# Performance work log

Hardware: AMD Instinct MI355X
Metric: run time of the kernel (lower is better)

Reference implementation:

```python
import jax, jax.numpy as jnp
import numpy as np
from jax import lax

N_NODES = 100_000
N_EDGES = 1_600_000
IN_CH = 128


def setup_inputs():
    key = jax.random.key(0)
    kx, ks, kd, kw, kb = jax.random.split(key, 5)
    x = jax.random.normal(kx, (N_NODES, IN_CH), dtype=jnp.float32)
    src = jax.random.randint(ks, (N_EDGES,), 0, N_NODES)
    dst = jax.random.randint(kd, (N_EDGES,), 0, N_NODES)
    # symmetrize (undirected graph, as PyG datasets typically are)
    edge_index = jnp.stack([jnp.concatenate([src, dst]),
                            jnp.concatenate([dst, src])])
    batch = jnp.sort(jax.random.randint(kb, (N_NODES,), 0, 8)).astype(jnp.int32)
    # mapper: Linear(in_channels, 1) params
    W = (jax.random.normal(kw, (IN_CH, 1), dtype=jnp.float32) / np.sqrt(IN_CH))
    b = jnp.zeros((1,), dtype=jnp.float32)
    return {"x": x, "W": W, "b": b, "edge_index": edge_index, "batch": batch}


def _forward(x, W, b, edge_index, batch):
    N = x.shape[0]
    elev = (x @ W + b)[:, 0]          # [N] per-node elevation (mapper)
    # clustering is discrete: stop gradients through the topology decisions
    elev_sg = lax.stop_gradient(elev)

    src, dst = edge_index[0], edge_index[1]
    E = src.shape[0]

    # --- peak / trough detection (self-loops satisfy both >= and <=) ---
    ones = jnp.ones((E,), dtype=jnp.int32)
    deg = jax.ops.segment_sum(ones, dst, num_segments=N)
    gt = (elev_sg[dst] >= elev_sg[src]).astype(jnp.int32)
    lt = (elev_sg[dst] <= elev_sg[src]).astype(jnp.int32)
    gt_sum = jax.ops.segment_sum(gt, dst, num_segments=N)
    lt_sum = jax.ops.segment_sum(lt, dst, num_segments=N)
    is_peak = gt_sum == deg        # node >= all its neighbors
    is_trough = lt_sum == deg      # node <= all its neighbors

    # --- watershed flood-fill: propagate peak ids along non-increasing edges ---
    down = elev_sg[dst] <= elev_sg[src]
    node_ids = jnp.arange(N)
    assign0 = jnp.where(is_peak, node_ids, -1)
    SENT = N  # sentinel for segment_min

    def body(state):
        assign, _ = state
        cand = jnp.where(down & (assign[src] >= 0) & (assign[dst] < 0),
                         assign[src], SENT)
        best = jax.ops.segment_min(cand, dst, num_segments=N)
        new = jnp.where((assign < 0) & (best < SENT), best, assign)
        return new, jnp.any(new != assign)

    assign, _ = lax.while_loop(lambda s: s[1], body,
                               (assign0, jnp.array(True)))

    # --- relabel peak-node ids to contiguous [0, K) (K = num peaks) ---
    new_id = jnp.cumsum(is_peak.astype(jnp.int32)) - 1
    assigned = assign >= 0
    seg = jnp.where(assigned, new_id[jnp.clip(assign, 0)], 0)  # [N] cluster id

    # --- scale: within-cluster softmax over elevation, weighted-sum pool ---
    NEG = jnp.float32(-1e30)
    e_m = jnp.where(assigned, elev, NEG)
    seg_max = jax.ops.segment_max(e_m, seg, num_segments=N)
    w = jnp.where(assigned, jnp.exp(elev - seg_max[seg]), 0.0)
    z = jax.ops.segment_sum(w, seg, num_segments=N)
    scaling = w / (z[seg] + 1e-12)
    pooled_x = jax.ops.segment_sum(x * scaling[:, None], seg, num_segments=N)  # [N,C], rows >= K are zero padding

    # --- per-cluster batch id = batch of the originating peak node ---
    cb_idx = jnp.where(is_peak, new_id, N)  # out-of-range dropped
    cluster_batch = jnp.full((N,), -1, dtype=batch.dtype).at[cb_idx].set(batch, mode='drop')

    return pooled_x, seg, scaling, cluster_batch, is_peak, is_trough


def reference(x, W, b, edge_index, batch):
    return _forward(x, W, b, edge_index, batch)
```

## Files before the change

### kernel.cpp

```cpp
#include <hip/hip_runtime.h>

#define SENT32 0x7FFFFFFF
#define IDMASK 0x1FFFF
#define RSHIFT 17
#define NLEVELS 8

__device__ __forceinline__ int block_alloc(int cnt, int* gctr, int* lds) {
    int lane = threadIdx.x & 63, wid = threadIdx.x >> 6;
    int pfx = cnt;
#pragma unroll
    for (int off = 1; off < 64; off <<= 1) {
        int t = __shfl_up(pfx, off, 64);
        if (lane >= off) pfx += t;
    }
    if (lane == 63) lds[wid] = pfx;
    __syncthreads();
    if (threadIdx.x == 0) {
        int t = lds[0] + lds[1] + lds[2] + lds[3];
        int bse = t ? atomicAdd(gctr, t) : 0;
        lds[4] = bse;
        lds[5] = bse + lds[0];
        lds[6] = lds[5] + lds[1];
        lds[7] = lds[6] + lds[2];
    }
    __syncthreads();
    return lds[4 + wid] + pfx - cnt;
}

__global__ __launch_bounds__(256) void k_matvec(const float* __restrict__ x,
                                                const float* __restrict__ W,
                                                const float* __restrict__ b,
                                                double* __restrict__ elev64,
                                                float* __restrict__ elev32,
                                                int N, int C) {
    int lane = threadIdx.x & 63;
    int wib  = threadIdx.x >> 6;
    int row  = blockIdx.x * (blockDim.x >> 6) + wib;
    if (row >= N) return;
    const float* xr = x + (size_t)row * C;
    double s = 0.0;
    for (int c = lane; c < C; c += 64) s += (double)xr[c] * (double)W[c];
#pragma unroll
    for (int off = 32; off > 0; off >>= 1) s += __shfl_down(s, off, 64);
    if (lane == 0) {
        double v = s + (double)b[0];
        elev64[row] = v;
        elev32[row] = (float)v;
    }
}

__global__ __launch_bounds__(256) void k_mark(const int* __restrict__ ei,
                                              const double* __restrict__ elev64,
                                              unsigned char* __restrict__ notpeak,
                                              unsigned char* __restrict__ nottrough,
                                              unsigned char* __restrict__ code,
                                              int Eh, int E) {
    int t0 = (blockIdx.x * 256 + threadIdx.x) * 4;
    if (t0 >= Eh) return;
    bool v0 = true, v1 = (t0 + 1 < Eh), v2 = (t0 + 2 < Eh), v3 = (t0 + 3 < Eh);
    int s0 = 0, s1 = 0, s2 = 0, s3 = 0, d0 = 0, d1 = 0, d2 = 0, d3 = 0;
    if (v3) {
        int4 sv = *(const int4*)&ei[t0];
        int4 dv = *(const int4*)&ei[(size_t)E + t0];
        s0 = sv.x; s1 = sv.y; s2 = sv.z; s3 = sv.w;
        d0 = dv.x; d1 = dv.y; d2 = dv.z; d3 = dv.w;
    } else {
        s0 = ei[t0];            d0 = ei[(size_t)E + t0];
        if (v1) { s1 = ei[t0 + 1]; d1 = ei[(size_t)E + t0 + 1]; }
        if (v2) { s2 = ei[t0 + 2]; d2 = ei[(size_t)E + t0 + 2]; }
    }
    double es0 = elev64[s0], es1 = elev64[s1], es2 = elev64[s2], es3 = elev64[s3];
    double ed0 = elev64[d0], ed1 = elev64[d1], ed2 = elev64[d2], ed3 = elev64[d3];
    unsigned cw = 0;
#define MARK1(J, VV, SS, DD, ES, ED)                                          \
    if (VV) {                                                                 \
        if (ED < ES)      { notpeak[DD] = 1; nottrough[SS] = 1; }             \
        else if (ED > ES) { notpeak[SS] = 1; nottrough[DD] = 1; }             \
        cw |= ((ED <= ES ? 1u : 0u) | (ES <= ED ? 2u : 0u)) << (8 * J);       \
    }
    MARK1(0, v0, s0, d0, es0, ed0)
    MARK1(1, v1, s1, d1, es1, ed1)
    MARK1(2, v2, s2, d2, es2, ed2)
    MARK1(3, v3, s3, d3, es3, ed3)
#undef MARK1
    if (v3) {
        *(unsigned*)&code[t0] = cw;
    } else {
        code[t0] = (unsigned char)(cw & 0xFF);
        if (v1) code[t0 + 1] = (unsigned char)((cw >> 8) & 0xFF);
        if (v2) code[t0 + 2] = (unsigned char)((cw >> 16) & 0xFF);
    }
}

__global__ __launch_bounds__(256) void k_nodes1(const unsigned char* __restrict__ notpeak,
                                                const unsigned char* __restrict__ nottrough,
                                                int* __restrict__ peakflag,
                                                int* __restrict__ best,
                                                unsigned char* __restrict__ rnd,
                                                float* __restrict__ out_ispeak,
                                                float* __restrict__ out_istrough,
                                                float* __restrict__ out_cb,
                                                int* __restrict__ part, int N) {
    __shared__ int ws[4];
    int n = blockIdx.x * 256 + threadIdx.x;
    int lane = threadIdx.x & 63, wid = threadIdx.x >> 6;
    int pk = 0;
    if (n < N) {
        pk = notpeak[n] ? 0 : 1;
        int tr = nottrough[n] ? 0 : 1;
        peakflag[n] = pk;
        out_ispeak[n] = (float)pk;
        out_istrough[n] = (float)tr;
        best[n] = pk ? n : SENT32;
        rnd[n] = pk ? 0 : 0xFF;
        out_cb[n] = -1.0f;
    }
    unsigned long long mk = __ballot(pk);
    if (lane == 0) ws[wid] = __popcll(mk);
    __syncthreads();
    if (threadIdx.x == 0) part[blockIdx.x] = ws[0] + ws[1] + ws[2] + ws[3];
}

__global__ __launch_bounds__(64) void k_scan_offs(const int* __restrict__ part,
                                                  int* __restrict__ offs, int P) {
    int lane = threadIdx.x;
    int chunk = (P + 63) / 64;
    int s0 = lane * chunk, s1 = min(s0 + chunk, P);
    int s = 0;
    for (int j = s0; j < s1; ++j) s += part[j];
    int incl = s;
#pragma unroll
    for (int off = 1; off < 64; off <<= 1) {
        int t = __shfl_up(incl, off, 64);
        if (lane >= off) incl += t;
    }
    int run = incl - s;
    for (int j = s0; j < s1; ++j) { offs[j] = run; run += part[j]; }
}

__global__ __launch_bounds__(256) void k_scan_final(const int* __restrict__ flag,
                                                    const int* __restrict__ offs,
                                                    int* __restrict__ out0, int N) {
    __shared__ int tmp[256];
    int n = blockIdx.x * 256 + threadIdx.x;
    int f = (n < N) ? flag[n] : 0;
    tmp[threadIdx.x] = f;
    __syncthreads();
    for (int off = 1; off < 256; off <<= 1) {
        int t = (threadIdx.x >= off) ? tmp[threadIdx.x - off] : 0;
        __syncthreads();
        tmp[threadIdx.x] += t;
        __syncthreads();
    }
    if (n < N) out0[n] = offs[blockIdx.x] + tmp[threadIdx.x] - 1;
}

__global__ __launch_bounds__(256) void k_build_l1(const int* __restrict__ ei,
                                                  const unsigned char* __restrict__ code,
                                                  const unsigned char* __restrict__ notpeak,
                                                  int* __restrict__ best,
                                                  unsigned char* __restrict__ rnd,
                                                  int Eh, int E) {
    int t0 = (blockIdx.x * 256 + threadIdx.x) * 4;
    if (t0 >= Eh) return;
    bool v0 = true, v1 = (t0 + 1 < Eh), v2 = (t0 + 2 < Eh), v3 = (t0 + 3 < Eh);
    int s0 = 0, s1 = 0, s2 = 0, s3 = 0, d0 = 0, d1 = 0, d2 = 0, d3 = 0;
    unsigned cw = 0;
    if (v3) {
        int4 sv = *(const int4*)&ei[t0];
        int4 dv = *(const int4*)&ei[(size_t)E + t0];
        s0 = sv.x; s1 = sv.y; s2 = sv.z; s3 = sv.w;
        d0 = dv.x; d1 = dv.y; d2 = dv.z; d3 = dv.w;
        cw = *(const unsigned*)&code[t0];
    } else {
        s0 = ei[t0];            d0 = ei[(size_t)E + t0];
        cw = (unsigned)code[t0];
        if (v1) { s1 = ei[t0 + 1]; d1 = ei[(size_t)E + t0 + 1];
                  cw |= (unsigned)code[t0 + 1] << 8; }
        if (v2) { s2 = ei[t0 + 2]; d2 = ei[(size_t)E + t0 + 2];
                  cw |= (unsigned)code[t0 + 2] << 16; }
    }
    unsigned char np_s0 = notpeak[s0], np_s1 = notpeak[s1],
                  np_s2 = notpeak[s2], np_s3 = notpeak[s3];
    unsigned char np_d0 = notpeak[d0], np_d1 = notpeak[d1],
                  np_d2 = notpeak[d2], np_d3 = notpeak[d3];
#define BUILD1(J, VV, SS, DD, NPS, NPD)                                       \
    if (VV) {                                                                 \
        unsigned cd = (cw >> (8 * J)) & 0xFFu;                                \
        bool ps = !NPS, pd = !NPD;                                            \
        if ((cd & 1u) && ps && !pd) {                                         \
            int old = atomicMin(&best[DD], (1 << RSHIFT) | SS);               \
            if (old == SENT32) rnd[DD] = 1;                                   \
        }                                                                     \
        if ((cd & 2u) && pd && !ps) {                                         \
            int old = atomicMin(&best[SS], (1 << RSHIFT) | DD);               \
            if (old == SENT32) rnd[SS] = 1;                                   \
        }                                                                     \
    }
    BUILD1(0, v0, s0, d0, np_s0, np_d0)
    BUILD1(1, v1, s1, d1, np_s1, np_d1)
    BUILD1(2, v2, s2, d2, np_s2, np_d2)
    BUILD1(3, v3, s3, d3, np_s3, np_d3)
#undef BUILD1
}

__global__ __launch_bounds__(256) void k_snap(const int* __restrict__ best,
                                              int* __restrict__ bsnap, int N) {
    int n = blockIdx.x * 256 + threadIdx.x;
    if (n < N) bsnap[n] = best[n];
}

__global__ __launch_bounds__(256) void k_sweep2(const int* __restrict__ ei,
                                                const unsigned char* __restrict__ code,
                                                const int* __restrict__ bsnap,
                                                int* __restrict__ best,
                                                unsigned char* __restrict__ rnd,
                                                int2* __restrict__ dst,
                                                int* __restrict__ dcnt,
                                                int Eh, int E) {
    __shared__ int lds[8];
    int t0 = (blockIdx.x * 256 + threadIdx.x) * 4;
    bool in = (t0 < Eh);
    bool v0 = in, v1 = (t0 + 1 < Eh), v2 = (t0 + 2 < Eh), v3 = (t0 + 3 < Eh);
    int s0 = 0, s1 = 0, s2 = 0, s3 = 0, d0 = 0, d1 = 0, d2 = 0, d3 = 0;
    unsigned cw = 0;
    if (v3) {
        int4 sv = *(const int4*)&ei[t0];
        int4 dv = *(const int4*)&ei[(size_t)E + t0];
        s0 = sv.x; s1 = sv.y; s2 = sv.z; s3 = sv.w;
        d0 = dv.x; d1 = dv.y; d2 = dv.z; d3 = dv.w;
        cw = *(const unsigned*)&code[t0];
    } else if (in) {
        s0 = ei[t0];            d0 = ei[(size_t)E + t0];
        cw = (unsigned)code[t0];
        if (v1) { s1 = ei[t0 + 1]; d1 = ei[(size_t)E + t0 + 1];
                  cw |= (unsigned)code[t0 + 1] << 8; }
        if (v2) { s2 = ei[t0 + 2]; d2 = ei[(size_t)E + t0 + 2];
                  cw |= (unsigned)code[t0 + 2] << 16; }
    }
    unsigned char rs0 = rnd[s0], rs1 = rnd[s1], rs2 = rnd[s2], rs3 = rnd[s3];
    unsigned char rd0 = rnd[d0], rd1 = rnd[d1], rd2 = rnd[d2], rd3 = rnd[d3];
    bool ka0 = false, ka1 = false, ka2 = false, ka3 = false;
    bool kb0 = false, kb1 = false, kb2 = false, kb3 = false;
    int cnt = 0;
#define SWEEP1(J, VV, SS, DD, RS, RD, KA, KB)                                 \
    if (VV) {                                                                 \
        unsigned cd = (cw >> (8 * J)) & 0xFFu;                                \
        if (cd & 1u) {                                                        \
            if (RS == 1) {                                                    \
                if (RD >= 2) {                                                \
                    int old = atomicMin(&best[DD], bsnap[SS] + (1 << RSHIFT));\
                    if (old == SENT32) rnd[DD] = 2;                           \
                }                                                             \
            } else if (RS != 0 && RD == 0xFF) { KA = true; ++cnt; }           \
        }                                                                     \
        if (cd & 2u) {                                                        \
            if (RD == 1) {                                                    \
                if (RS >= 2) {                                                \
                    int old = atomicMin(&best[SS], bsnap[DD] + (1 << RSHIFT));\
                    if (old == SENT32) rnd[SS] = 2;                           \
                }                                                             \
            } else if (RD != 0 && RS == 0xFF) { KB = true; ++cnt; }           \
        }                                                                     \
    }
    SWEEP1(0, v0, s0, d0, rs0, rd0, ka0, kb0)
    SWEEP1(1, v1, s1, d1, rs1, rd1, ka1, kb1)
    SWEEP1(2, v2, s2, d2, rs2, rd2, ka2, kb2)
    SWEEP1(3, v3, s3, d3, rs3, rd3, ka3, kb3)
#undef SWEEP1
    int base = block_alloc(cnt, &dcnt[2], lds);
    if (ka0) dst[base++] = make_int2(s0, d0);
    if (kb0) dst[base++] = make_int2(d0, s0);
    if (ka1) dst[base++] = make_int2(s1, d1);
    if (kb1) dst[base++] = make_int2(d1, s1);
    if (ka2) dst[base++] = make_int2(s2, d2);
    if (kb2) dst[base++] = make_int2(d2, s2);
    if (ka3) dst[base++] = make_int2(s3, d3);
    if (kb3) dst[base]   = make_int2(d3, s3);
}

__global__ __launch_bounds__(256) void k_level_e(int2* __restrict__ d0p,
                                                 int2* __restrict__ d1p,
                                                 int* __restrict__ dcnt,
                                                 int* __restrict__ best,
                                                 unsigned char* __restrict__ rnd,
                                                 int L) {
    int ne = dcnt[L - 1];
    if (ne == 0) return;
    const int2* src = ((L - 1) & 1) ? d1p : d0p;
    int2* dst = (L & 1) ? d1p : d0p;
    __shared__ int lds[8];
    const unsigned char Lf = (unsigned char)(L - 1), Lc = (unsigned char)L;
    int stride = gridDim.x * 1024;
    for (int base = blockIdx.x * 1024; base < ne; base += stride) {
        int i0 = base + threadIdx.x * 4;
        int2 e0 = make_int2(0, 0), e1 = e0, e2 = e0, e3 = e0;
        bool v0 = (i0 < ne), v1 = (i0 + 1 < ne), v2 = (i0 + 2 < ne), v3 = (i0 + 3 < ne);
        if (v3) {
            int4 a = *(const int4*)&src[i0];
            int4 b2 = *(const int4*)&src[i0 + 2];
            e0 = make_int2(a.x, a.y);   e1 = make_int2(a.z, a.w);
            e2 = make_int2(b2.x, b2.y); e3 = make_int2(b2.z, b2.w);
        } else {
            if (v0) e0 = src[i0];
            if (v1) e1 = src[i0 + 1];
            if (v2) e2 = src[i0 + 2];
        }
        unsigned char rs0 = rnd[e0.x], rs1 = rnd[e1.x], rs2 = rnd[e2.x], rs3 = rnd[e3.x];
        unsigned char rd0 = rnd[e0.y], rd1 = rnd[e1.y], rd2 = rnd[e2.y], rd3 = rnd[e3.y];
        bool k0 = false, k1 = false, k2 = false, k3 = false;
        int cnt = 0;
#define LEVEL1(VV, EE, RS, RD, KK)                                            \
    if (VV) {                                                                 \
        if (RS == Lf) {                                                       \
            if (RD >= Lc) {                                                   \
                int old = atomicMin(&best[EE.y], best[EE.x] + (1 << RSHIFT)); \
                if (old == SENT32) rnd[EE.y] = Lc;                            \
            }                                                                 \
        } else if (RD == 0xFF) { KK = true; ++cnt; }                          \
    }
        LEVEL1(v0, e0, rs0, rd0, k0)
        LEVEL1(v1, e1, rs1, rd1, k1)
        LEVEL1(v2, e2, rs2, rd2, k2)
        LEVEL1(v3, e3, rs3, rd3, k3)
#undef LEVEL1
        int wbase = block_alloc(cnt, &dcnt[L], lds);
        if (k0) dst[wbase++] = e0;
        if (k1) dst[wbase++] = e1;
        if (k2) dst[wbase++] = e2;
        if (k3) dst[wbase]   = e3;
        __syncthreads();
    }
}

__global__ __launch_bounds__(1024) void k_tail_e(int2* __restrict__ d0p,
                                                 int2* __restrict__ d1p,
                                                 int* __restrict__ dcnt,
                                                 int* __restrict__ best) {
    for (int L = NLEVELS + 1; L < 2000; ++L) {
        int ne = dcnt[L - 1];
        if (ne == 0) return;
        const int2* src = ((L - 1) & 1) ? d1p : d0p;
        int2* dst = (L & 1) ? d1p : d0p;
        for (int i = threadIdx.x; i < ne; i += blockDim.x) {
            int2 ed = src[i];
            int bs = best[ed.x];
            if ((bs >> RSHIFT) == L - 1) {
                int cand = bs + (1 << RSHIFT);
                if (best[ed.y] > cand) atomicMin(&best[ed.y], cand);
            } else if (best[ed.y] == SENT32) {
                int pos = atomicAdd(&dcnt[L], 1);
                dst[pos] = ed;
            }
        }
        __threadfence();
        __syncthreads();
    }
}

__global__ __launch_bounds__(256) void k_segw(const int* __restrict__ best,
                                              const int* __restrict__ new_id,
                                              const float* __restrict__ elev32,
                                              const int* __restrict__ batch,
                                              int* __restrict__ seg,
                                              float* __restrict__ out_seg,
                                              float* __restrict__ out_cb,
                                              float* __restrict__ wbuf,
                                              float* __restrict__ z, int N) {
    int n = blockIdx.x * blockDim.x + threadIdx.x;
    if (n >= N) return;
    int a = best[n];
    int sg = 0;
    float wv = 0.0f;
    if (a != SENT32) {
        int pk = a & IDMASK;
        sg = new_id[pk];
        if ((a >> RSHIFT) == 0) out_cb[sg] = (float)batch[n];
        wv = expf(elev32[n] - elev32[pk]);
        atomicAdd(&z[sg], wv);
    }
    seg[n] = sg;
    out_seg[n] = (float)sg;
    wbuf[n] = wv;
}

__global__ __launch_bounds__(256) void k_pool(const float* __restrict__ x,
                                              const int* __restrict__ seg,
                                              const float* __restrict__ wbuf,
                                              const float* __restrict__ z,
                                              float* __restrict__ out_scaling,
                                              float* __restrict__ out_pooled,
                                              int N, int C) {
    int lane = threadIdx.x & 63;
    int node = blockIdx.x * (blockDim.x >> 6) + (threadIdx.x >> 6);
    if (node >= N) return;
    int sg = seg[node];
    float sc = wbuf[node] / (z[sg] + 1e-12f);
    if (lane == 0) out_scaling[node] = sc;
    const float* xr = x + (size_t)node * C;
    float* pr = out_pooled + (size_t)sg * C;
    for (int c = lane; c < C; c += 64) atomicAdd(&pr[c], xr[c] * sc);
}

extern "C" void kernel_launch(void* const* d_in, const int* in_sizes, int n_in,
                              void* d_out, int out_size, void* d_ws, size_t ws_size,
                              hipStream_t stream) {
    const float* x = (const float*)d_in[0];
    const float* W = (const float*)d_in[1];
    const float* b = (const float*)d_in[2];
    const int* ei = (const int*)d_in[3];
    const int* batch = (const int*)d_in[4];

    const int C = in_sizes[1];
    const int N = in_sizes[0] / C;
    const int E = in_sizes[3] / 2;
    const int Eh = E / 2;

    float* out_pooled   = (float*)d_out;
    float* out_seg      = out_pooled + (size_t)N * C;
    float* out_scaling  = out_seg + N;
    float* out_cb       = out_scaling + N;
    float* out_ispeak   = out_cb + N;
    float* out_istrough = out_ispeak + N;

    char* p = (char*)d_ws;
    auto alloc = [&](size_t bytes) -> char* {
        char* r = p;
        p += (bytes + 255) & ~(size_t)255;
        return r;
    };
    double* elev64 = (double*)alloc((size_t)N * 8);
    float* elev32  = (float*)alloc((size_t)N * 4);
    int* best      = (int*)alloc((size_t)N * 4);
    int* bsnap     = (int*)alloc((size_t)N * 4);
    int* peakflag  = (int*)alloc((size_t)N * 4);
    int* new_id    = (int*)alloc((size_t)N * 4);
    int* seg       = (int*)alloc((size_t)N * 4);
    float* wbuf    = (float*)alloc((size_t)N * 4);
    unsigned char* rnd = (unsigned char*)alloc((size_t)N);
    const int P = (N + 255) / 256;
    int* part = (int*)alloc((size_t)P * 4);
    int* offs = (int*)alloc((size_t)P * 4);
    unsigned char* code = (unsigned char*)alloc((size_t)Eh);
    char* zbeg = p;
    unsigned char* notpeak   = (unsigned char*)alloc((size_t)N);
    unsigned char* nottrough = (unsigned char*)alloc((size_t)N);
    float* z   = (float*)alloc((size_t)N * 4);
    int* dcnt  = (int*)alloc(2048 * 4);
    size_t zspan = (size_t)(p - zbeg);
    int2* down0 = (int2*)alloc((size_t)E * 8);
    int2* down1 = (int2*)alloc((size_t)E * 8);
    (void)ws_size;

    hipMemsetAsync(zbeg, 0, zspan, stream);
    hipMemsetAsync(out_pooled, 0, (size_t)N * C * sizeof(float), stream);

    const int B4 = (Eh + 1023) / 1024;

    k_matvec<<<(N + 3) / 4, 256, 0, stream>>>(x, W, b, elev64, elev32, N, C);
    k_mark<<<B4, 256, 0, stream>>>(ei, elev64, notpeak, nottrough, code, Eh, E);
    k_nodes1<<<P, 256, 0, stream>>>(notpeak, nottrough, peakflag, best, rnd,
                                    out_ispeak, out_istrough, out_cb, part, N);
    k_scan_offs<<<1, 64, 0, stream>>>(part, offs, P);
    k_scan_final<<<P, 256, 0, stream>>>(peakflag, offs, new_id, N);

    k_build_l1<<<B4, 256, 0, stream>>>(ei, code, notpeak, best, rnd, Eh, E);
    k_snap<<<P, 256, 0, stream>>>(best, bsnap, N);
    k_sweep2<<<B4, 256, 0, stream>>>(ei, code, bsnap, best, rnd, down0, dcnt, Eh, E);

    for (int L = 3; L <= NLEVELS; ++L)
        k_level_e<<<2048, 256, 0, stream>>>(down0, down1, dcnt, best, rnd, L);
    k_tail_e<<<1, 1024, 0, stream>>>(down0, down1, dcnt, best);

    k_segw<<<(N + 255) / 256, 256, 0, stream>>>(best, new_id, elev32, batch, seg,
                                                out_seg, out_cb, wbuf, z, N);
    k_pool<<<(N + 3) / 4, 256, 0, stream>>>(x, seg, wbuf, z, out_scaling,
                                            out_pooled, N, C);
}
```

Measured before the change: 245.7 us.

## Counting-sort nodes by cluster before atomic pooling to localize atomics

Adds a per-cluster histogram in the segment-weight kernel, a prefix scan over it, and a fill kernel that writes node indices grouped by cluster. The pooling kernel then walks nodes in cluster order, so consecutive wavefronts issue atomics to the same output row. The aim is better cache locality and atomic coalescing on the pooled output. The cost is four extra launches, extra global atomics for the histogram and fill, and x rows being read in scattered order instead of sequentially.

```diff
diff --git a/kernel.cpp b/kernel.cpp
--- a/kernel.cpp
+++ b/kernel.cpp
@@ -121,6 +121,19 @@
     if (threadIdx.x == 0) part[blockIdx.x] = ws[0] + ws[1] + ws[2] + ws[3];
 }
 
+__global__ __launch_bounds__(256) void k_scan_part(const int* __restrict__ flag,
+                                                   int* __restrict__ part, int N) {
+    int n = blockIdx.x * 256 + threadIdx.x;
+    int f = (n < N) ? flag[n] : 0;
+#pragma unroll
+    for (int off = 32; off > 0; off >>= 1) f += __shfl_down(f, off, 64);
+    __shared__ int ws[4];
+    int lane = threadIdx.x & 63, wid = threadIdx.x >> 6;
+    if (lane == 0) ws[wid] = f;
+    __syncthreads();
+    if (threadIdx.x == 0) part[blockIdx.x] = ws[0] + ws[1] + ws[2] + ws[3];
+}
+
 __global__ __launch_bounds__(64) void k_scan_offs(const int* __restrict__ part,
                                                   int* __restrict__ offs, int P) {
     int lane = threadIdx.x;
@@ -140,7 +153,9 @@
 
 __global__ __launch_bounds__(256) void k_scan_final(const int* __restrict__ flag,
                                                     const int* __restrict__ offs,
-                                                    int* __restrict__ out0, int N) {
+                                                    int* __restrict__ out0,
+                                                    int* __restrict__ out1,
+                                                    int mode, int N) {
     __shared__ int tmp[256];
     int n = blockIdx.x * 256 + threadIdx.x;
     int f = (n < N) ? flag[n] : 0;
@@ -152,7 +167,16 @@
         tmp[threadIdx.x] += t;
         __syncthreads();
     }
-    if (n < N) out0[n] = offs[blockIdx.x] + tmp[threadIdx.x] - 1;
+    if (n < N) {
+        int incl = offs[blockIdx.x] + tmp[threadIdx.x];
+        if (mode == 0) {
+            out0[n] = incl - 1;
+        } else {
+            int excl = incl - f;
+            out0[n] = excl;
+            out1[n] = excl;
+        }
+    }
 }
 
 __global__ __launch_bounds__(256) void k_build_l1(const int* __restrict__ ei,
@@ -366,7 +390,8 @@
                                               float* __restrict__ out_seg,
                                               float* __restrict__ out_cb,
                                               float* __restrict__ wbuf,
-                                              float* __restrict__ z, int N) {
+                                              float* __restrict__ z,
+                                              int* __restrict__ hist, int N) {
     int n = blockIdx.x * blockDim.x + threadIdx.x;
     if (n >= N) return;
     int a = best[n];
@@ -382,18 +407,30 @@
     seg[n] = sg;
     out_seg[n] = (float)sg;
     wbuf[n] = wv;
-}
-
-__global__ __launch_bounds__(256) void k_pool(const float* __restrict__ x,
-                                              const int* __restrict__ seg,
-                                              const float* __restrict__ wbuf,
-                                              const float* __restrict__ z,
-                                              float* __restrict__ out_scaling,
-                                              float* __restrict__ out_pooled,
-                                              int N, int C) {
+    atomicAdd(&hist[sg], 1);
+}
+
+__global__ __launch_bounds__(256) void k_cfill(const int* __restrict__ seg,
+                                               int* __restrict__ ccursor,
+                                               int* __restrict__ members, int N) {
+    int n = blockIdx.x * blockDim.x + threadIdx.x;
+    if (n >= N) return;
+    int pos = atomicAdd(&ccursor[seg[n]], 1);
+    members[pos] = n;
+}
+
+__global__ __launch_bounds__(256) void k_pool_m(const float* __restrict__ x,
+                                                const int* __restrict__ members,
+                                                const int* __restrict__ seg,
+                                                const float* __restrict__ wbuf,
+                                                const float* __restrict__ z,
+                                                float* __restrict__ out_scaling,
+                                                float* __restrict__ out_pooled,
+                                                int N, int C) {
     int lane = threadIdx.x & 63;
-    int node = blockIdx.x * (blockDim.x >> 6) + (threadIdx.x >> 6);
-    if (node >= N) return;
+    int i = blockIdx.x * (blockDim.x >> 6) + (threadIdx.x >> 6);
+    if (i >= N) return;
+    int node = members[i];
     int sg = seg[node];
     float sc = wbuf[node] / (z[sg] + 1e-12f);
     if (lane == 0) out_scaling[node] = sc;
@@ -437,6 +474,9 @@
     int* new_id    = (int*)alloc((size_t)N * 4);
     int* seg       = (int*)alloc((size_t)N * 4);
     float* wbuf    = (float*)alloc((size_t)N * 4);
+    int* members   = (int*)alloc((size_t)N * 4);
+    int* cstart    = (int*)alloc((size_t)N * 4);
+    int* ccursor   = (int*)alloc((size_t)N * 4);
     unsigned char* rnd = (unsigned char*)alloc((size_t)N);
     const int P = (N + 255) / 256;
     int* part = (int*)alloc((size_t)P * 4);
@@ -446,6 +486,7 @@
     unsigned char* notpeak   = (unsigned char*)alloc((size_t)N);
     unsigned char* nottrough = (unsigned char*)alloc((size_t)N);
     float* z   = (float*)alloc((size_t)N * 4);
+    int* hist  = (int*)alloc((size_t)N * 4);
     int* dcnt  = (int*)alloc(2048 * 4);
     size_t zspan = (size_t)(p - zbeg);
     int2* down0 = (int2*)alloc((size_t)E * 8);
@@ -462,7 +503,7 @@
     k_nodes1<<<P, 256, 0, stream>>>(notpeak, nottrough, peakflag, best, rnd,
                                     out_ispeak, out_istrough, out_cb, part, N);
     k_scan_offs<<<1, 64, 0, stream>>>(part, offs, P);
-    k_scan_final<<<P, 256, 0, stream>>>(peakflag, offs, new_id, N);
+    k_scan_final<<<P, 256, 0, stream>>>(peakflag, offs, new_id, nullptr, 0, N);
 
     k_build_l1<<<B4, 256, 0, stream>>>(ei, code, notpeak, best, rnd, Eh, E);
     k_snap<<<P, 256, 0, stream>>>(best, bsnap, N);
@@ -473,7 +514,12 @@
     k_tail_e<<<1, 1024, 0, stream>>>(down0, down1, dcnt, best);
 
     k_segw<<<(N + 255) / 256, 256, 0, stream>>>(best, new_id, elev32, batch, seg,
-                                                out_seg, out_cb, wbuf, z, N);
-    k_pool<<<(N + 3) / 4, 256, 0, stream>>>(x, seg, wbuf, z, out_scaling,
-                                            out_pooled, N, C);
-}
+                                                out_seg, out_cb, wbuf, z, hist, N);
+    k_scan_part<<<P, 256, 0, stream>>>(hist, part, N);
+    k_scan_offs<<<1, 64, 0, stream>>>(part, offs, P);
+    k_scan_final<<<P, 256, 0, stream>>>(hist, offs, cstart, ccursor, 1, N);
+    k_cfill<<<(N + 255) / 256, 256, 0, stream>>>(seg, ccursor, members, N);
+
+    k_pool_m<<<(N + 3) / 4, 256, 0, stream>>>(x, members, seg, wbuf, z,
+                                              out_scaling, out_pooled, N, C);
+}
```

Result: slower. 298.3 us (+21.4%).
